# Kernel optimization log

Measured on AMD Instinct MI355X. Metric: run time of the kernel, lower is better.

## Reference

```python
import jax, jax.numpy as jnp
import numpy as np
import math

D_MODEL = 2048
NUM_HEADS = 16
D_HEAD = D_MODEL // NUM_HEADS
ROPE_BASE = 10000.0

def _rope(t, pos):
    # t: [b, h, T, d_head]; standard rotate-half RoPE with base 10000.
    T, d = t.shape[-2], t.shape[-1]
    start = max(pos, 0)  # pos < 0 means training / position 0
    inv_freq = 1.0 / (ROPE_BASE ** (jnp.arange(0, d, 2, dtype=jnp.float32) / d))  # [d/2]
    positions = jnp.arange(start, start + T, dtype=jnp.float32)                   # [T]
    ang = positions[:, None] * inv_freq[None, :]                                  # [T, d/2]
    cos, sin = jnp.cos(ang), jnp.sin(ang)
    x1, x2 = t[..., : d // 2], t[..., d // 2 :]
    return jnp.concatenate([x1 * cos - x2 * sin, x1 * sin + x2 * cos], axis=-1)

def setup_inputs() -> dict:
    key = jax.random.key(0)
    kx, kq, kk, kv, kw = jax.random.split(key, 5)
    s = 1.0 / math.sqrt(D_MODEL)
    return {
        "x": jax.random.normal(kx, (2, 2048, D_MODEL), dtype=jnp.float32),
        "q_out": jax.random.normal(kq, (D_MODEL, D_MODEL), dtype=jnp.float32) * s,
        "k_out": jax.random.normal(kk, (D_MODEL, D_MODEL), dtype=jnp.float32) * s,
        "v_out": jax.random.normal(kv, (D_MODEL, D_MODEL), dtype=jnp.float32) * s,
        "w_out": jax.random.normal(kw, (D_MODEL, D_MODEL), dtype=jnp.float32) * s,
        "pos": 0,
    }

def reference(x, q_out, k_out, v_out, w_out, pos):
    b, t, d = x.shape
    h, dh = NUM_HEADS, D_HEAD

    def heads(y):  # [b, t, d] -> [b, h, t, dh]
        return y.reshape(b, t, h, dh).transpose(0, 2, 1, 3)

    q = _rope(heads(jnp.einsum('btd,de->bte', x, q_out)), pos)
    k = _rope(heads(jnp.einsum('btd,de->bte', x, k_out)), pos)
    v = heads(jnp.einsum('btd,de->bte', x, v_out))

    score = jnp.einsum('bhqd,bhkd->bhqk', q, k) / math.sqrt(dh)
    causal = jnp.triu(jnp.ones((t, t), dtype=bool), k=1)  # True above diagonal -> masked
    score = jnp.where(causal, -jnp.inf, score)
    weights = jax.nn.softmax(score, axis=-1)
    ctx = jnp.einsum('bhqk,bhkd->bhqd', weights, v)        # [b, h, t, dh]
    ctx = ctx.transpose(0, 2, 1, 3).reshape(b, t, d)
    return jnp.einsum('btd,de->bte', ctx, w_out)
```

## Files before the change

### kernel.cpp

```cpp
#include <hip/hip_runtime.h>
#include <hip/hip_bf16.h>
#include <math.h>

#define NH 16
#define DH 128
#define DM 2048
#define BB 2
#define TT 2048

typedef unsigned short u16;
typedef __attribute__((ext_vector_type(8))) __bf16 bf16x8;
typedef __attribute__((ext_vector_type(8))) u16 u16x8;
typedef __attribute__((ext_vector_type(4))) u16 u16x4;
typedef __attribute__((ext_vector_type(4))) float f32x4;

__device__ __forceinline__ float bf2f(u16 a){
  union { unsigned u; float f; } v; v.u = ((unsigned)a) << 16; return v.f;
}
__device__ __forceinline__ u16 f2bf(float f){
  union { float f; unsigned u; } v; v.f = f;
  unsigned r = v.u + 0x7fffu + ((v.u >> 16) & 1u);
  return (u16)(r >> 16);
}

typedef const __attribute__((address_space(1))) unsigned int* gas_p;
typedef __attribute__((address_space(3))) unsigned int* las_p;
__device__ __forceinline__ void gl_lds16(const u16* g, u16* lds_uniform_base){
  __builtin_amdgcn_global_load_lds((gas_p)(const void*)g,
                                   (las_p)(void*)lds_uniform_base, 16, 0, 0);
}

__global__ __launch_bounds__(256)
void cvt_f32_bf16(const float* __restrict__ src, u16* __restrict__ dst, int n4){
  const int i = blockIdx.x * 256 + threadIdx.x;
  if (i >= n4) return;
  const f32x4 v = *(const f32x4*)(src + (size_t)i * 4);
  u16x4 o;
  #pragma unroll
  for (int j = 0; j < 4; j++) o[j] = f2bf(v[j]);
  *(u16x4*)(dst + (size_t)i * 4) = o;
}

__global__ __launch_bounds__(256)
void transpose2048(const float* __restrict__ W, u16* __restrict__ Wt){
  __shared__ u16 tile[32][33];
  const int tx = threadIdx.x, ty = threadIdx.y;
  const int bx = blockIdx.x * 32, by = blockIdx.y * 32;
  #pragma unroll
  for (int i = 0; i < 32; i += 8)
    tile[ty + i][tx] = f2bf(W[(size_t)(by + ty + i) * DM + bx + tx]);
  __syncthreads();
  #pragma unroll
  for (int i = 0; i < 32; i += 8)
    Wt[(size_t)(bx + ty + i) * DM + by + tx] = tile[tx][ty + i];
}

__global__ __launch_bounds__(256)
void transpose3(const float* __restrict__ w0, const float* __restrict__ w1,
                const float* __restrict__ w2, u16* __restrict__ dst){
  __shared__ u16 tile[32][33];
  const int z = blockIdx.z;
  const float* W = (z == 0) ? w0 : (z == 1) ? w1 : w2;
  u16* Wt = dst + (size_t)z * DM * DM;
  const int tx = threadIdx.x, ty = threadIdx.y;
  const int bx = blockIdx.x * 32, by = blockIdx.y * 32;
  #pragma unroll
  for (int i = 0; i < 32; i += 8)
    tile[ty + i][tx] = f2bf(W[(size_t)(by + ty + i) * DM + bx + tx]);
  __syncthreads();
  #pragma unroll
  for (int i = 0; i < 32; i += 8)
    Wt[(size_t)(bx + ty + i) * DM + by + tx] = tile[tx][ty + i];
}

__global__ __launch_bounds__(256)
void gemm_bt(const u16* __restrict__ A, const u16* __restrict__ Bt_base,
             void* __restrict__ C0, u16* __restrict__ Ck, u16* __restrict__ Cv,
             int mode0){
  __shared__ u16 As[2][128][32];
  __shared__ u16 Bs[2][128][32];
  const int z = blockIdx.z;
  const u16* Bt = Bt_base + (size_t)z * DM * DM;
  void* C = (z == 0) ? C0 : (z == 1) ? (void*)Ck : (void*)Cv;
  const int mode = (z == 0) ? mode0 : (z == 1) ? 3 : 2;

  const int tid = threadIdx.x;
  const int wave = tid >> 6, lane = tid & 63;
  const int wm = wave & 1, wn = wave >> 1;
  const int row16 = lane & 15, quad = lane >> 4;
  const int m0 = blockIdx.x * 128, n0 = blockIdx.y * 128;

  const f32x4 zero = {0.f, 0.f, 0.f, 0.f};
  f32x4 acc[4][4];
  #pragma unroll
  for (int i = 0; i < 4; i++)
    #pragma unroll
    for (int j = 0; j < 4; j++) acc[i][j] = zero;

  const int srow = lane >> 2;
  const int scol = (lane & 3) * 8;

  for (int k0 = 0; k0 < DM; k0 += 64){
    #pragma unroll
    for (int c = 0; c < 2; c++){
      const int rbase = wave * 32 + c * 16;
      const u16* pa = A  + (size_t)(m0 + rbase + srow) * DM + k0 + scol;
      const u16* pb = Bt + (size_t)(n0 + rbase + srow) * DM + k0 + scol;
      gl_lds16(pa,      &As[0][rbase][0]);
      gl_lds16(pa + 32, &As[1][rbase][0]);
      gl_lds16(pb,      &Bs[0][rbase][0]);
      gl_lds16(pb + 32, &Bs[1][rbase][0]);
    }
    __syncthreads();
    #pragma unroll
    for (int buf = 0; buf < 2; buf++){
      bf16x8 af[4], bfr[4];
      #pragma unroll
      for (int mt = 0; mt < 4; mt++)
        af[mt] = *(const bf16x8*)&As[buf][wm * 64 + mt * 16 + row16][quad * 8];
      #pragma unroll
      for (int nt = 0; nt < 4; nt++)
        bfr[nt] = *(const bf16x8*)&Bs[buf][wn * 64 + nt * 16 + row16][quad * 8];
      #pragma unroll
      for (int mt = 0; mt < 4; mt++)
        #pragma unroll
        for (int nt = 0; nt < 4; nt++)
          acc[mt][nt] = __builtin_amdgcn_mfma_f32_16x16x32_bf16(af[mt], bfr[nt], acc[mt][nt], 0, 0, 0);
    }
    __syncthreads();
  }

  #pragma unroll
  for (int mt = 0; mt < 4; mt++){
    #pragma unroll
    for (int nt = 0; nt < 4; nt++){
      #pragma unroll
      for (int r = 0; r < 4; r++){
        const int m = m0 + wm * 64 + mt * 16 + quad * 4 + r;
        const int n = n0 + wn * 64 + nt * 16 + row16;
        const int b = m >> 11, t = m & (TT - 1);
        const int hh = n >> 7, dh = n & (DH - 1);
        if (mode == 1){
          ((u16*)C)[(((size_t)(b * NH + hh) * TT + t) * DH) + dh] = f2bf(acc[mt][nt][r]);
        } else if (mode == 3){
          const int dhs = dh ^ ((t & 7) << 3);
          ((u16*)C)[(((size_t)(b * NH + hh) * TT + t) * DH) + dhs] = f2bf(acc[mt][nt][r]);
        } else if (mode == 2){
          const int ts = (t & 63) ^ ((dh & 7) << 3);
          ((u16*)C)[(((size_t)(b * NH + hh) * 32 + (t >> 6)) * 8192) + dh * 64 + ts] = f2bf(acc[mt][nt][r]);
        } else {
          ((float*)C)[(size_t)m * DM + n] = acc[mt][nt][r];
        }
      }
    }
  }
}

__global__ __launch_bounds__(256)
void rope2(u16* __restrict__ qb, u16* __restrict__ kb, const int* __restrict__ posp){
  const int idx = blockIdx.x * 256 + threadIdx.x;
  const int pair = idx & 63;
  const int row = idx >> 6;
  const int t = row & (TT - 1);
  int p0 = *posp; if (p0 < 0) p0 = 0;
  const float tf = (float)(p0 + t);
  const size_t base = (size_t)row * DH;
  {
    const float inv = expf(-(float)pair * (9.2103403719761836f / 64.f));
    float sn, cs; sincosf(tf * inv, &sn, &cs);
    const float q1 = bf2f(qb[base + pair]);
    const float q2 = bf2f(qb[base + 64 + pair]);
    qb[base + pair]      = f2bf(q1 * cs - q2 * sn);
    qb[base + 64 + pair] = f2bf(q1 * sn + q2 * cs);
  }
  {
    const int pl = pair ^ ((t & 7) << 3);
    const float inv = expf(-(float)pl * (9.2103403719761836f / 64.f));
    float sn, cs; sincosf(tf * inv, &sn, &cs);
    const float k1 = bf2f(kb[base + pair]);
    const float k2 = bf2f(kb[base + 64 + pair]);
    kb[base + pair]      = f2bf(k1 * cs - k2 * sn);
    kb[base + 64 + pair] = f2bf(k1 * sn + k2 * cs);
  }
}

template<bool MASK>
__device__ __forceinline__ void attn_tile(
    int kt0, int qbase, int wave, int row16, int quad,
    const bf16x8 (&qf)[4],
    u16 (&k_s)[64][128], u16 (&vt_s)[128][64], u16 (&p_s)[4][16][72],
    f32x4 (&o_acc)[8], float (&l_acc)[4])
{
  const float scale = 0.08838834764831845f;
  const f32x4 zero = {0.f, 0.f, 0.f, 0.f};
  const int fx = (row16 & 7) << 3;
  f32x4 s_acc[4];
  #pragma unroll
  for (int nt = 0; nt < 4; nt++) s_acc[nt] = zero;
  #pragma unroll
  for (int st = 0; st < 4; st++)
    #pragma unroll
    for (int nt = 0; nt < 4; nt++){
      const bf16x8 kf = *(const bf16x8*)&k_s[nt * 16 + row16][(st * 32 + quad * 8) ^ fx];
      s_acc[nt] = __builtin_amdgcn_mfma_f32_16x16x32_bf16(qf[st], kf, s_acc[nt], 0, 0, 0);
    }
  #pragma unroll
  for (int r = 0; r < 4; r++){
    float ps = 0.f;
    #pragma unroll
    for (int nt = 0; nt < 4; nt++){
      float p = __expf(s_acc[nt][r] * scale);
      if (MASK){
        const int qr = qbase + quad * 4 + r;
        if (kt0 + nt * 16 + row16 > qr) p = 0.f;
      }
      ps += p;
      p_s[wave][quad * 4 + r][nt * 16 + row16] = f2bf(p);
    }
    l_acc[r] += ps;
  }
  asm volatile("" ::: "memory");

  #pragma unroll
  for (int kk = 0; kk < 2; kk++){
    const bf16x8 pf = *(const bf16x8*)&p_s[wave][row16][kk * 32 + quad * 8];
    #pragma unroll
    for (int nd = 0; nd < 8; nd++){
      const bf16x8 vb = *(const bf16x8*)&vt_s[nd * 16 + row16][(kk * 32 + quad * 8) ^ fx];
      o_acc[nd] = __builtin_amdgcn_mfma_f32_16x16x32_bf16(pf, vb, o_acc[nd], 0, 0, 0);
    }
  }
}

__global__ __launch_bounds__(256)
void attn_fwd(const u16* __restrict__ q, const u16* __restrict__ k,
              const u16* __restrict__ vtg, u16* __restrict__ ctx){
  __shared__ u16 k_s[64][128];
  __shared__ u16 vt_s[128][64];
  __shared__ u16 p_s[4][16][72];
  const int tid = threadIdx.x;
  const int wave = tid >> 6, lane = tid & 63;
  const int row16 = lane & 15, quad = lane >> 4;
  const int bh = blockIdx.y;
  const int q0 = (31 - blockIdx.x) * 64;
  const int qbase = q0 + wave * 16;
  const size_t bho = (size_t)bh * TT * DH;

  bf16x8 qf[4];
  {
    const u16* qp = q + bho + (size_t)(qbase + row16) * DH + quad * 8;
    #pragma unroll
    for (int st = 0; st < 4; st++) qf[st] = *(const bf16x8*)(qp + st * 32);
  }

  float l_acc[4] = {0.f, 0.f, 0.f, 0.f};
  const f32x4 zero = {0.f, 0.f, 0.f, 0.f};
  f32x4 o_acc[8];
  #pragma unroll
  for (int i = 0; i < 8; i++) o_acc[i] = zero;

  const int kl_r = lane >> 4, kl_c = (lane & 15) * 8;
  const int vl_r = lane >> 3, vl_c = (lane & 7) * 8;

  for (int kt0 = 0; kt0 < q0 + 64; kt0 += 64){
    #pragma unroll
    for (int i = 0; i < 4; i++){
      const int rb = wave * 16 + i * 4;
      gl_lds16(k + bho + (size_t)(kt0 + rb + kl_r) * DH + kl_c, &k_s[rb][0]);
    }
    const u16* vpan = vtg + ((size_t)bh * 32 + (kt0 >> 6)) * 8192;
    #pragma unroll
    for (int i = 0; i < 4; i++){
      const int rb = wave * 32 + i * 8;
      gl_lds16(vpan + (size_t)(rb + vl_r) * 64 + vl_c, &vt_s[rb][0]);
    }
    __syncthreads();

    if (kt0 < q0)
      attn_tile<false>(kt0, qbase, wave, row16, quad, qf, k_s, vt_s, p_s, o_acc, l_acc);
    else
      attn_tile<true >(kt0, qbase, wave, row16, quad, qf, k_s, vt_s, p_s, o_acc, l_acc);

    __syncthreads();
  }

  #pragma unroll
  for (int r = 0; r < 4; r++){
    #pragma unroll
    for (int off = 1; off < 16; off <<= 1) l_acc[r] += __shfl_xor(l_acc[r], off, 64);
  }

  const int b = bh >> 4, h = bh & 15;
  #pragma unroll
  for (int nd = 0; nd < 8; nd++){
    #pragma unroll
    for (int r = 0; r < 4; r++){
      const int qr = qbase + quad * 4 + r;
      const size_t off = ((size_t)b * TT + qr) * DM + h * DH + nd * 16 + row16;
      ctx[off] = f2bf(o_acc[nd][r] / l_acc[r]);
    }
  }
}

extern "C" void kernel_launch(void* const* d_in, const int* in_sizes, int n_in,
                              void* d_out, int out_size, void* d_ws, size_t ws_size,
                              hipStream_t stream){
  const float* x  = (const float*)d_in[0];
  const float* wq = (const float*)d_in[1];
  const float* wk = (const float*)d_in[2];
  const float* wv = (const float*)d_in[3];
  const float* wo = (const float*)d_in[4];
  const int* pos  = (const int*)d_in[5];

  char* ws = (char*)d_ws;
  const dim3 tg(64, 64), tb(32, 8);

  if (ws_size >= 92274688ull){
    u16* xb  = (u16*)ws;                  u16* cb = xb;
    u16* wt3 = (u16*)(ws + 16777216);
    u16* qb  = (u16*)(ws + 41943040);
    u16* kb  = (u16*)(ws + 58720256);
    u16* vtg = (u16*)(ws + 75497472);

    cvt_f32_bf16<<<8192, 256, 0, stream>>>(x, xb, 2097152);
    transpose3<<<dim3(64, 64, 3), tb, 0, stream>>>(wq, wk, wv, wt3);
    gemm_bt<<<dim3(32, 16, 3), 256, 0, stream>>>(xb, wt3, qb, kb, vtg, 1);
    transpose2048<<<tg, tb, 0, stream>>>(wo, wt3);
    rope2<<<16384, 256, 0, stream>>>(qb, kb, pos);
    attn_fwd<<<dim3(32, 32), 256, 0, stream>>>(qb, kb, vtg, cb);
    gemm_bt<<<dim3(32, 16, 1), 256, 0, stream>>>(cb, wt3, d_out, 0, 0, 0);
  } else {
    u16* xb  = (u16*)ws;                  u16* cb = xb;
    u16* wt  = (u16*)(ws + 16777216);
    u16* qb  = (u16*)(ws + 25165824);
    u16* kb  = (u16*)(ws + 41943040);
    u16* vtg = (u16*)(ws + 58720256);

    cvt_f32_bf16<<<8192, 256, 0, stream>>>(x, xb, 2097152);
    transpose2048<<<tg, tb, 0, stream>>>(wq, wt);
    gemm_bt<<<dim3(32, 16, 1), 256, 0, stream>>>(xb, wt, qb, 0, 0, 1);
    transpose2048<<<tg, tb, 0, stream>>>(wk, wt);
    gemm_bt<<<dim3(32, 16, 1), 256, 0, stream>>>(xb, wt, kb, 0, 0, 3);
    transpose2048<<<tg, tb, 0, stream>>>(wv, wt);
    gemm_bt<<<dim3(32, 16, 1), 256, 0, stream>>>(xb, wt, vtg, 0, 0, 2);
    rope2<<<16384, 256, 0, stream>>>(qb, kb, pos);
    attn_fwd<<<dim3(32, 32), 256, 0, stream>>>(qb, kb, vtg, cb);
    transpose2048<<<tg, tb, 0, stream>>>(wo, wt);
    gemm_bt<<<dim3(32, 16, 1), 256, 0, stream>>>(cb, wt, d_out, 0, 0, 0);
  }
}
```

Measured before the change: 458.8 us.

## Add 256x256-tile pipelined GEMM kernel for fused QKV projection

Adds a new gemm256 kernel with 512 threads and 256x256 output tiles. It double-buffers K-slices in LDS using direct global-to-LDS loads, interleaved with MFMA phases, explicit vmcnt waits, barriers and setprio. The fused QKV projection now uses it instead of the older 128-tile gemm_bt. The aim is more data reuse per tile and better overlap of loads with MFMA compute. The cost is higher register and LDS pressure and fewer blocks (384) to fill the GPU.

```diff
diff --git a/kernel.cpp b/kernel.cpp
--- a/kernel.cpp
+++ b/kernel.cpp
@@ -156,6 +156,123 @@
   }
 }
 
+#define SB() do{ asm volatile("" ::: "memory"); \
+                 __builtin_amdgcn_s_barrier();  \
+                 asm volatile("" ::: "memory"); }while(0)
+#define WAITV4 asm volatile("s_waitcnt vmcnt(4)" ::: "memory")
+#define WAITV0 asm volatile("s_waitcnt vmcnt(0)" ::: "memory")
+#define NOPW do{}while(0)
+
+#define STAGE_A(bf, kh, koff) do{ \
+  gl_lds16(aS + (koff),                    &As[bf][kh][wave * 16][0]); \
+  gl_lds16(aS + (size_t)128 * DM + (koff), &As[bf][kh][128 + wave * 16][0]); }while(0)
+#define STAGE_B(bf, kh, koff) do{ \
+  gl_lds16(bS + (koff),                    &Bs[bf][kh][wave * 16][0]); \
+  gl_lds16(bS + (size_t)128 * DM + (koff), &Bs[bf][kh][128 + wave * 16][0]); }while(0)
+
+#define PHASE(bufc, kh, fh, STAGE, WAIT) do{ \
+  bf16x8 af[4]; \
+  _Pragma("unroll") \
+  for (int i = 0; i < 4; i++) \
+    af[i] = *(const bf16x8*)&As[bufc][kh][wm * 128 + (fh) * 64 + i * 16 + row16][quad * 8]; \
+  if ((fh) == 0){ \
+    _Pragma("unroll") \
+    for (int j = 0; j < 4; j++) \
+      bk[j] = *(const bf16x8*)&Bs[bufc][kh][wn * 64 + j * 16 + row16][quad * 8]; \
+  } \
+  STAGE; WAIT; \
+  SB(); \
+  __builtin_amdgcn_s_setprio(1); \
+  _Pragma("unroll") \
+  for (int i = 0; i < 4; i++) \
+    _Pragma("unroll") \
+    for (int j = 0; j < 4; j++) \
+      acc[(fh) * 4 + i][j] = __builtin_amdgcn_mfma_f32_16x16x32_bf16(af[i], bk[j], acc[(fh) * 4 + i][j], 0, 0, 0); \
+  __builtin_amdgcn_s_setprio(0); \
+  SB(); \
+}while(0)
+
+__global__ __launch_bounds__(512, 2)
+void gemm256(const u16* __restrict__ A, const u16* __restrict__ Bt_base,
+             void* __restrict__ C0, u16* __restrict__ Ck, u16* __restrict__ Cv,
+             int mode0){
+  __shared__ u16 As[2][2][256][32];
+  __shared__ u16 Bs[2][2][256][32];
+  const int z = blockIdx.z;
+  const u16* Bt = Bt_base + (size_t)z * DM * DM;
+  void* C = (z == 0) ? C0 : (z == 1) ? (void*)Ck : (void*)Cv;
+  const int mode = (z == 0) ? mode0 : (z == 1) ? 3 : 2;
+
+  const int tid = threadIdx.x;
+  const int wave = tid >> 6, lane = tid & 63;
+  const int wm = wave >> 2, wn = wave & 3;
+  const int row16 = lane & 15, quad = lane >> 4;
+  const int m0 = blockIdx.x * 256, n0 = blockIdx.y * 256;
+
+  const int srow = wave * 16 + (lane >> 2);
+  const int scol = (lane & 3) * 8;
+  const u16* aS = A  + (size_t)(m0 + srow) * DM + scol;
+  const u16* bS = Bt + (size_t)(n0 + srow) * DM + scol;
+
+  const f32x4 zero = {0.f, 0.f, 0.f, 0.f};
+  f32x4 acc[8][4];
+  #pragma unroll
+  for (int i = 0; i < 8; i++)
+    #pragma unroll
+    for (int j = 0; j < 4; j++) acc[i][j] = zero;
+  bf16x8 bk[4];
+
+  STAGE_A(0, 0, 0);  STAGE_B(0, 0, 0);
+  STAGE_A(0, 1, 32); STAGE_B(0, 1, 32);
+  STAGE_A(1, 0, 64); STAGE_B(1, 0, 64);
+  WAITV4;
+  SB();
+
+  #pragma unroll 2
+  for (int t = 0; t < 30; ++t){
+    const int buf = t & 1, nb = buf ^ 1;
+    const int k1 = (t + 1) * 64 + 32;
+    const int k2 = (t + 2) * 64;
+    PHASE(buf, 0, 0, STAGE_A(nb, 1, k1), NOPW);
+    PHASE(buf, 0, 1, STAGE_B(nb, 1, k1), NOPW);
+    PHASE(buf, 1, 0, STAGE_A(buf, 0, k2), NOPW);
+    PHASE(buf, 1, 1, STAGE_B(buf, 0, k2), WAITV4);
+  }
+  PHASE(0, 0, 0, STAGE_A(1, 1, 31 * 64 + 32), NOPW);
+  PHASE(0, 0, 1, STAGE_B(1, 1, 31 * 64 + 32), NOPW);
+  PHASE(0, 1, 0, NOPW, NOPW);
+  PHASE(0, 1, 1, NOPW, WAITV0);
+  PHASE(1, 0, 0, NOPW, NOPW);
+  PHASE(1, 0, 1, NOPW, NOPW);
+  PHASE(1, 1, 0, NOPW, NOPW);
+  PHASE(1, 1, 1, NOPW, NOPW);
+
+  #pragma unroll
+  for (int mt = 0; mt < 8; mt++){
+    #pragma unroll
+    for (int nt = 0; nt < 4; nt++){
+      #pragma unroll
+      for (int r = 0; r < 4; r++){
+        const int m = m0 + wm * 128 + mt * 16 + quad * 4 + r;
+        const int n = n0 + wn * 64 + nt * 16 + row16;
+        const int b = m >> 11, t = m & (TT - 1);
+        const int hh = n >> 7, dh = n & (DH - 1);
+        if (mode == 1){
+          ((u16*)C)[(((size_t)(b * NH + hh) * TT + t) * DH) + dh] = f2bf(acc[mt][nt][r]);
+        } else if (mode == 3){
+          const int dhs = dh ^ ((t & 7) << 3);
+          ((u16*)C)[(((size_t)(b * NH + hh) * TT + t) * DH) + dhs] = f2bf(acc[mt][nt][r]);
+        } else if (mode == 2){
+          const int ts = (t & 63) ^ ((dh & 7) << 3);
+          ((u16*)C)[(((size_t)(b * NH + hh) * 32 + (t >> 6)) * 8192) + dh * 64 + ts] = f2bf(acc[mt][nt][r]);
+        } else {
+          ((float*)C)[(size_t)m * DM + n] = acc[mt][nt][r];
+        }
+      }
+    }
+  }
+}
+
 __global__ __launch_bounds__(256)
 void rope2(u16* __restrict__ qb, u16* __restrict__ kb, const int* __restrict__ posp){
   const int idx = blockIdx.x * 256 + threadIdx.x;
@@ -324,7 +441,7 @@
 
     cvt_f32_bf16<<<8192, 256, 0, stream>>>(x, xb, 2097152);
     transpose3<<<dim3(64, 64, 3), tb, 0, stream>>>(wq, wk, wv, wt3);
-    gemm_bt<<<dim3(32, 16, 3), 256, 0, stream>>>(xb, wt3, qb, kb, vtg, 1);
+    gemm256<<<dim3(16, 8, 3), 512, 0, stream>>>(xb, wt3, qb, kb, vtg, 1);
     transpose2048<<<tg, tb, 0, stream>>>(wo, wt3);
     rope2<<<16384, 256, 0, stream>>>(qb, kb, pos);
     attn_fwd<<<dim3(32, 32), 256, 0, stream>>>(qb, kb, vtg, cb);
```

New measurement: 485.1 us. 1.06x slower.

## Add double-buffered async-LDS GEMM with split-phase barriers and setprio

Applied to the files above, without the earlier changes.

Adds gemm_bt2, a GEMM kernel that double-buffers A/B tiles in LDS using global_load_lds. It issues the next k-chunk's loads before computing the current chunk and waits with explicit vmcnt counters. MFMA sections are wrapped in s_setprio to favour math waves. The goal is to overlap global memory latency with MFMA work in the QKV and output projections, at the cost of more LDS and hand-managed wait counts that must stay correct.

```diff
diff --git a/kernel.cpp b/kernel.cpp
--- a/kernel.cpp
+++ b/kernel.cpp
@@ -29,6 +29,12 @@
   __builtin_amdgcn_global_load_lds((gas_p)(const void*)g,
                                    (las_p)(void*)lds_uniform_base, 16, 0, 0);
 }
+
+#define SB() do{ asm volatile("" ::: "memory"); \
+                 __builtin_amdgcn_s_barrier();  \
+                 asm volatile("" ::: "memory"); }while(0)
+#define WAITV4 asm volatile("s_waitcnt vmcnt(4)" ::: "memory")
+#define WAITV0 asm volatile("s_waitcnt vmcnt(0)" ::: "memory")
 
 __global__ __launch_bounds__(256)
 void cvt_f32_bf16(const float* __restrict__ src, u16* __restrict__ dst, int n4){
@@ -157,6 +163,113 @@
 }
 
 __global__ __launch_bounds__(256)
+void gemm_bt2(const u16* __restrict__ A, const u16* __restrict__ Bt_base,
+              void* __restrict__ C0, u16* __restrict__ Ck, u16* __restrict__ Cv,
+              int mode0){
+  __shared__ u16 As[2][128][32];
+  __shared__ u16 Bs[2][128][32];
+  const int z = blockIdx.z;
+  const u16* Bt = Bt_base + (size_t)z * DM * DM;
+  void* C = (z == 0) ? C0 : (z == 1) ? (void*)Ck : (void*)Cv;
+  const int mode = (z == 0) ? mode0 : (z == 1) ? 3 : 2;
+
+  const int tid = threadIdx.x;
+  const int wave = tid >> 6, lane = tid & 63;
+  const int wm = wave & 1, wn = wave >> 1;
+  const int row16 = lane & 15, quad = lane >> 4;
+  const int m0 = blockIdx.x * 128, n0 = blockIdx.y * 128;
+
+  const f32x4 zero = {0.f, 0.f, 0.f, 0.f};
+  f32x4 acc[4][4];
+  #pragma unroll
+  for (int i = 0; i < 4; i++)
+    #pragma unroll
+    for (int j = 0; j < 4; j++) acc[i][j] = zero;
+
+  const int srow = lane >> 2;
+  const int scol = ((lane & 3) ^ ((lane >> 3) & 3)) * 8;
+  const u16* aBase = A  + (size_t)(m0 + wave * 32 + srow) * DM + scol;
+  const u16* bBase = Bt + (size_t)(n0 + wave * 32 + srow) * DM + scol;
+
+  const int fcol = (quad ^ ((row16 >> 1) & 3)) * 8;
+
+  #define STAGE2(kh, kc) do{ \
+    const int ko = (kc) + (kh) * 32; \
+    gl_lds16(aBase + ko,                     &As[kh][wave * 32][0]); \
+    gl_lds16(aBase + ko + (size_t)16 * DM,   &As[kh][wave * 32 + 16][0]); \
+    gl_lds16(bBase + ko,                     &Bs[kh][wave * 32][0]); \
+    gl_lds16(bBase + ko + (size_t)16 * DM,   &Bs[kh][wave * 32 + 16][0]); \
+  }while(0)
+
+  #define PHASE2(kh) do{ \
+    bf16x8 af[4], bk[4]; \
+    _Pragma("unroll") \
+    for (int mt = 0; mt < 4; mt++) \
+      af[mt] = *(const bf16x8*)&As[kh][wm * 64 + mt * 16 + row16][fcol]; \
+    _Pragma("unroll") \
+    for (int nt = 0; nt < 4; nt++) \
+      bk[nt] = *(const bf16x8*)&Bs[kh][wn * 64 + nt * 16 + row16][fcol]; \
+    __builtin_amdgcn_s_setprio(1); \
+    _Pragma("unroll") \
+    for (int mt = 0; mt < 4; mt++) \
+      _Pragma("unroll") \
+      for (int nt = 0; nt < 4; nt++) \
+        acc[mt][nt] = __builtin_amdgcn_mfma_f32_16x16x32_bf16(af[mt], bk[nt], acc[mt][nt], 0, 0, 0); \
+    __builtin_amdgcn_s_setprio(0); \
+  }while(0)
+
+  STAGE2(0, 0);
+
+  for (int t = 0; t < 31; ++t){
+    const int kc = t * 64;
+    STAGE2(1, kc);
+    WAITV4;
+    SB();
+    PHASE2(0);
+    SB();
+    STAGE2(0, kc + 64);
+    WAITV4;
+    SB();
+    PHASE2(1);
+    SB();
+  }
+  STAGE2(1, 31 * 64);
+  WAITV4; SB();
+  PHASE2(0);
+  SB();
+  WAITV0; SB();
+  PHASE2(1);
+
+  #undef STAGE2
+  #undef PHASE2
+
+  #pragma unroll
+  for (int mt = 0; mt < 4; mt++){
+    #pragma unroll
+    for (int nt = 0; nt < 4; nt++){
+      #pragma unroll
+      for (int r = 0; r < 4; r++){
+        const int m = m0 + wm * 64 + mt * 16 + quad * 4 + r;
+        const int n = n0 + wn * 64 + nt * 16 + row16;
+        const int b = m >> 11, t = m & (TT - 1);
+        const int hh = n >> 7, dh = n & (DH - 1);
+        if (mode == 1){
+          ((u16*)C)[(((size_t)(b * NH + hh) * TT + t) * DH) + dh] = f2bf(acc[mt][nt][r]);
+        } else if (mode == 3){
+          const int dhs = dh ^ ((t & 7) << 3);
+          ((u16*)C)[(((size_t)(b * NH + hh) * TT + t) * DH) + dhs] = f2bf(acc[mt][nt][r]);
+        } else if (mode == 2){
+          const int ts = (t & 63) ^ ((dh & 7) << 3);
+          ((u16*)C)[(((size_t)(b * NH + hh) * 32 + (t >> 6)) * 8192) + dh * 64 + ts] = f2bf(acc[mt][nt][r]);
+        } else {
+          ((float*)C)[(size_t)m * DM + n] = acc[mt][nt][r];
+        }
+      }
+    }
+  }
+}
+
+__global__ __launch_bounds__(256)
 void rope2(u16* __restrict__ qb, u16* __restrict__ kb, const int* __restrict__ posp){
   const int idx = blockIdx.x * 256 + threadIdx.x;
   const int pair = idx & 63;
@@ -324,11 +437,11 @@
 
     cvt_f32_bf16<<<8192, 256, 0, stream>>>(x, xb, 2097152);
     transpose3<<<dim3(64, 64, 3), tb, 0, stream>>>(wq, wk, wv, wt3);
-    gemm_bt<<<dim3(32, 16, 3), 256, 0, stream>>>(xb, wt3, qb, kb, vtg, 1);
+    gemm_bt2<<<dim3(32, 16, 3), 256, 0, stream>>>(xb, wt3, qb, kb, vtg, 1);
     transpose2048<<<tg, tb, 0, stream>>>(wo, wt3);
     rope2<<<16384, 256, 0, stream>>>(qb, kb, pos);
     attn_fwd<<<dim3(32, 32), 256, 0, stream>>>(qb, kb, vtg, cb);
-    gemm_bt<<<dim3(32, 16, 1), 256, 0, stream>>>(cb, wt3, d_out, 0, 0, 0);
+    gemm_bt2<<<dim3(32, 16, 1), 256, 0, stream>>>(cb, wt3, d_out, 0, 0, 0);
   } else {
     u16* xb  = (u16*)ws;                  u16* cb = xb;
     u16* wt  = (u16*)(ws + 16777216);
```

Measured after the change: 475.9 us. 1.04x slower.

## Triple-buffer GEMM LDS staging with swizzle and raise MFMA priority

Applied to the files above, without the earlier changes.

Replaces the GEMM's load-then-sync loop with a three-stage ring of LDS buffers. Global-to-LDS loads for two k-steps ahead are issued while MFMAs consume the current one, gated by vmcnt waits and a single barrier per phase. It also XOR-swizzles the LDS column placement to reduce bank conflicts on fragment reads, and wraps MFMA blocks in both GEMM and attention with s_setprio. The cost is more LDS per block, which may lower occupancy, plus hand-managed wait counts that must exactly match the number of loads in flight.

```diff
diff --git a/kernel.cpp b/kernel.cpp
--- a/kernel.cpp
+++ b/kernel.cpp
@@ -29,6 +29,12 @@
   __builtin_amdgcn_global_load_lds((gas_p)(const void*)g,
                                    (las_p)(void*)lds_uniform_base, 16, 0, 0);
 }
+
+#define SB() do{ asm volatile("" ::: "memory"); \
+                 __builtin_amdgcn_s_barrier();  \
+                 asm volatile("" ::: "memory"); }while(0)
+#define WAITV4 asm volatile("s_waitcnt vmcnt(4)" ::: "memory")
+#define WAITV0 asm volatile("s_waitcnt vmcnt(0)" ::: "memory")
 
 __global__ __launch_bounds__(256)
 void cvt_f32_bf16(const float* __restrict__ src, u16* __restrict__ dst, int n4){
@@ -74,11 +80,11 @@
 }
 
 __global__ __launch_bounds__(256)
-void gemm_bt(const u16* __restrict__ A, const u16* __restrict__ Bt_base,
-             void* __restrict__ C0, u16* __restrict__ Ck, u16* __restrict__ Cv,
-             int mode0){
-  __shared__ u16 As[2][128][32];
-  __shared__ u16 Bs[2][128][32];
+void gemm_bt3(const u16* __restrict__ A, const u16* __restrict__ Bt_base,
+              void* __restrict__ C0, u16* __restrict__ Ck, u16* __restrict__ Cv,
+              int mode0){
+  __shared__ u16 As[3][128][32];
+  __shared__ u16 Bs[3][128][32];
   const int z = blockIdx.z;
   const u16* Bt = Bt_base + (size_t)z * DM * DM;
   void* C = (z == 0) ? C0 : (z == 1) ? (void*)Ck : (void*)Cv;
@@ -98,37 +104,57 @@
     for (int j = 0; j < 4; j++) acc[i][j] = zero;
 
   const int srow = lane >> 2;
-  const int scol = (lane & 3) * 8;
-
-  for (int k0 = 0; k0 < DM; k0 += 64){
-    #pragma unroll
-    for (int c = 0; c < 2; c++){
-      const int rbase = wave * 32 + c * 16;
-      const u16* pa = A  + (size_t)(m0 + rbase + srow) * DM + k0 + scol;
-      const u16* pb = Bt + (size_t)(n0 + rbase + srow) * DM + k0 + scol;
-      gl_lds16(pa,      &As[0][rbase][0]);
-      gl_lds16(pa + 32, &As[1][rbase][0]);
-      gl_lds16(pb,      &Bs[0][rbase][0]);
-      gl_lds16(pb + 32, &Bs[1][rbase][0]);
-    }
-    __syncthreads();
-    #pragma unroll
-    for (int buf = 0; buf < 2; buf++){
-      bf16x8 af[4], bfr[4];
-      #pragma unroll
-      for (int mt = 0; mt < 4; mt++)
-        af[mt] = *(const bf16x8*)&As[buf][wm * 64 + mt * 16 + row16][quad * 8];
-      #pragma unroll
-      for (int nt = 0; nt < 4; nt++)
-        bfr[nt] = *(const bf16x8*)&Bs[buf][wn * 64 + nt * 16 + row16][quad * 8];
-      #pragma unroll
-      for (int mt = 0; mt < 4; mt++)
-        #pragma unroll
-        for (int nt = 0; nt < 4; nt++)
-          acc[mt][nt] = __builtin_amdgcn_mfma_f32_16x16x32_bf16(af[mt], bfr[nt], acc[mt][nt], 0, 0, 0);
-    }
-    __syncthreads();
-  }
+  const int scol = ((lane & 3) ^ ((lane >> 3) & 3)) * 8;
+  const u16* aBase = A  + (size_t)(m0 + wave * 32 + srow) * DM + scol;
+  const u16* bBase = Bt + (size_t)(n0 + wave * 32 + srow) * DM + scol;
+
+  const int fcol = (quad ^ ((row16 >> 1) & 3)) * 8;
+
+  #define STG3(bs, ko) do{ \
+    gl_lds16(aBase + (ko),                   &As[bs][wave * 32][0]); \
+    gl_lds16(aBase + (ko) + 16 * DM,         &As[bs][wave * 32 + 16][0]); \
+    gl_lds16(bBase + (ko),                   &Bs[bs][wave * 32][0]); \
+    gl_lds16(bBase + (ko) + 16 * DM,         &Bs[bs][wave * 32 + 16][0]); \
+  }while(0)
+
+  #define CMP3(bc) do{ \
+    bf16x8 af[4], bk[4]; \
+    _Pragma("unroll") \
+    for (int mt = 0; mt < 4; mt++) \
+      af[mt] = *(const bf16x8*)&As[bc][wm * 64 + mt * 16 + row16][fcol]; \
+    _Pragma("unroll") \
+    for (int nt = 0; nt < 4; nt++) \
+      bk[nt] = *(const bf16x8*)&Bs[bc][wn * 64 + nt * 16 + row16][fcol]; \
+    __builtin_amdgcn_s_setprio(1); \
+    _Pragma("unroll") \
+    for (int mt = 0; mt < 4; mt++) \
+      _Pragma("unroll") \
+      for (int nt = 0; nt < 4; nt++) \
+        acc[mt][nt] = __builtin_amdgcn_mfma_f32_16x16x32_bf16(af[mt], bk[nt], acc[mt][nt], 0, 0, 0); \
+    __builtin_amdgcn_s_setprio(0); \
+  }while(0)
+
+  #define PH3S(bc, bs, ko) do{ WAITV4; SB(); STG3(bs, ko); CMP3(bc); }while(0)
+  #define PH3N(bc, WAIT)   do{ WAIT;   SB();               CMP3(bc); }while(0)
+
+  STG3(0, 0);
+  STG3(1, 32);
+
+  int ko = 64;
+  for (int i = 0; i < 20; ++i){
+    PH3S(0, 2, ko); ko += 32;
+    PH3S(1, 0, ko); ko += 32;
+    PH3S(2, 1, ko); ko += 32;
+  }
+  PH3S(0, 2, ko); ko += 32;
+  PH3S(1, 0, ko);
+  PH3N(2, WAITV4);
+  PH3N(0, WAITV0);
+
+  #undef PH3S
+  #undef PH3N
+  #undef STG3
+  #undef CMP3
 
   #pragma unroll
   for (int mt = 0; mt < 4; mt++){
@@ -197,6 +223,7 @@
   f32x4 s_acc[4];
   #pragma unroll
   for (int nt = 0; nt < 4; nt++) s_acc[nt] = zero;
+  __builtin_amdgcn_s_setprio(1);
   #pragma unroll
   for (int st = 0; st < 4; st++)
     #pragma unroll
@@ -204,6 +231,7 @@
       const bf16x8 kf = *(const bf16x8*)&k_s[nt * 16 + row16][(st * 32 + quad * 8) ^ fx];
       s_acc[nt] = __builtin_amdgcn_mfma_f32_16x16x32_bf16(qf[st], kf, s_acc[nt], 0, 0, 0);
     }
+  __builtin_amdgcn_s_setprio(0);
   #pragma unroll
   for (int r = 0; r < 4; r++){
     float ps = 0.f;
@@ -221,6 +249,7 @@
   }
   asm volatile("" ::: "memory");
 
+  __builtin_amdgcn_s_setprio(1);
   #pragma unroll
   for (int kk = 0; kk < 2; kk++){
     const bf16x8 pf = *(const bf16x8*)&p_s[wave][row16][kk * 32 + quad * 8];
@@ -230,6 +259,7 @@
       o_acc[nd] = __builtin_amdgcn_mfma_f32_16x16x32_bf16(pf, vb, o_acc[nd], 0, 0, 0);
     }
   }
+  __builtin_amdgcn_s_setprio(0);
 }
 
 __global__ __launch_bounds__(256)
@@ -324,11 +354,11 @@
 
     cvt_f32_bf16<<<8192, 256, 0, stream>>>(x, xb, 2097152);
     transpose3<<<dim3(64, 64, 3), tb, 0, stream>>>(wq, wk, wv, wt3);
-    gemm_bt<<<dim3(32, 16, 3), 256, 0, stream>>>(xb, wt3, qb, kb, vtg, 1);
+    gemm_bt3<<<dim3(32, 16, 3), 256, 0, stream>>>(xb, wt3, qb, kb, vtg, 1);
     transpose2048<<<tg, tb, 0, stream>>>(wo, wt3);
     rope2<<<16384, 256, 0, stream>>>(qb, kb, pos);
     attn_fwd<<<dim3(32, 32), 256, 0, stream>>>(qb, kb, vtg, cb);
-    gemm_bt<<<dim3(32, 16, 1), 256, 0, stream>>>(cb, wt3, d_out, 0, 0, 0);
+    gemm_bt3<<<dim3(32, 16, 1), 256, 0, stream>>>(cb, wt3, d_out, 0, 0, 0);
   } else {
     u16* xb  = (u16*)ws;                  u16* cb = xb;
     u16* wt  = (u16*)(ws + 16777216);
@@ -338,14 +368,14 @@
 
     cvt_f32_bf16<<<8192, 256, 0, stream>>>(x, xb, 2097152);
     transpose2048<<<tg, tb, 0, stream>>>(wq, wt);
-    gemm_bt<<<dim3(32, 16, 1), 256, 0, stream>>>(xb, wt, qb, 0, 0, 1);
+    gemm_bt3<<<dim3(32, 16, 1), 256, 0, stream>>>(xb, wt, qb, 0, 0, 1);
     transpose2048<<<tg, tb, 0, stream>>>(wk, wt);
-    gemm_bt<<<dim3(32, 16, 1), 256, 0, stream>>>(xb, wt, kb, 0, 0, 3);
+    gemm_bt3<<<dim3(32, 16, 1), 256, 0, stream>>>(xb, wt, kb, 0, 0, 3);
     transpose2048<<<tg, tb, 0, stream>>>(wv, wt);
-    gemm_bt<<<dim3(32, 16, 1), 256, 0, stream>>>(xb, wt, vtg, 0, 0, 2);
+    gemm_bt3<<<dim3(32, 16, 1), 256, 0, stream>>>(xb, wt, vtg, 0, 0, 2);
     rope2<<<16384, 256, 0, stream>>>(qb, kb, pos);
     attn_fwd<<<dim3(32, 32), 256, 0, stream>>>(qb, kb, vtg, cb);
     transpose2048<<<tg, tb, 0, stream>>>(wo, wt);
-    gemm_bt<<<dim3(32, 16, 1), 256, 0, stream>>>(cb, wt, d_out, 0, 0, 0);
-  }
-}
+    gemm_bt3<<<dim3(32, 16, 1), 256, 0, stream>>>(cb, wt, d_out, 0, 0, 0);
+  }
+}
```

New measurement: 482.5 us. +5.2%, slower.
